# Performance work log

Measured on AMD Instinct MI355X. Metric: run time of the kernel, lower is better.

The kernel has to match this reference:

```python
import jax, jax.numpy as jnp
import numpy as np

SLOPE = 0.01  # LeakyReLU default negative slope


def grid_sample2d(image, grid):
    """Bilinear, padding_mode='border', align_corners=True.
    image: [B,C,H,W], grid: [B,h,w,2] in [-1,1]. Returns [B,C,h,w]."""
    B, C, H, W = image.shape
    _, h, w, _ = grid.shape
    ix = (grid[..., 0] + 1) / 2 * (W - 1)  # [B,h,w]
    iy = (grid[..., 1] + 1) / 2 * (H - 1)
    ix0 = jnp.floor(ix)
    iy0 = jnp.floor(iy)
    # bilinear weights (computed from unclamped corner coords, as in source)
    nw = (ix0 + 1 - ix) * (iy0 + 1 - iy)
    ne = (ix - ix0) * (iy0 + 1 - iy)
    sw = (ix0 + 1 - ix) * (iy - iy0)
    se = (ix - ix0) * (iy - iy0)
    x0 = jnp.clip(ix0.astype(jnp.int32), 0, W - 1)
    x1 = jnp.clip(ix0.astype(jnp.int32) + 1, 0, W - 1)
    y0 = jnp.clip(iy0.astype(jnp.int32), 0, H - 1)
    y1 = jnp.clip(iy0.astype(jnp.int32) + 1, 0, H - 1)
    img = image.reshape(B, C, H * W)

    def gather(yi, xi):
        idx = (yi * W + xi).reshape(B, 1, h * w)
        idx = jnp.broadcast_to(idx, (B, C, h * w))
        return jnp.take_along_axis(img, idx, axis=2).reshape(B, C, h, w)

    out = (gather(y0, x0) * nw[:, None] + gather(y0, x1) * ne[:, None]
           + gather(y1, x0) * sw[:, None] + gather(y1, x1) * se[:, None])
    return out


def leaky_relu(x):
    return jnp.where(x >= 0, x, SLOPE * x)


def setup_inputs() -> dict:
    key = jax.random.key(0)
    ks = jax.random.split(key, 10)
    B, C, H, W = 1, 32, 512, 512
    h, w = 2048, 512
    hid, out_dim = 32, 4
    inp = {
        "xy": jax.random.normal(ks[0], (B, C, H, W), jnp.float32),
        "xz": jax.random.normal(ks[1], (B, C, H, W), jnp.float32),
        "yz": jax.random.normal(ks[2], (B, C, H, W), jnp.float32),
        "coords": jax.random.uniform(ks[3], (B, h, w, 3), jnp.float32, -1.0, 1.0),
        "gauss_mat": jax.random.normal(ks[4], (3, 16), jnp.float32),
        "W0": jax.random.normal(ks[5], (C + 32, C), jnp.float32) * 0.1,
        "b0": jnp.zeros((C,), jnp.float32),
        "W1": jax.random.normal(ks[6], (C, hid), jnp.float32) * 0.1,
        "b1": jnp.zeros((hid,), jnp.float32),
        "W2": jax.random.normal(ks[7], (hid, hid), jnp.float32) * 0.1,
        "b2": jnp.zeros((hid,), jnp.float32),
        "W3": jax.random.normal(ks[8], (hid, out_dim), jnp.float32) * 0.1,
        "b3": jnp.zeros((out_dim,), jnp.float32),
    }
    return inp


def reference(xy, xz, yz, coords, gauss_mat, W0, b0, W1, b1, W2, b2, W3, b3):
    e1 = grid_sample2d(xy, coords[..., jnp.array([0, 1])])
    e2 = grid_sample2d(xz, coords[..., jnp.array([0, 2])])
    e3 = grid_sample2d(yz, coords[..., jnp.array([1, 2])])
    x = (e1 + e2 + e3) / 3.0  # [B,C,h,w]
    x = jnp.moveaxis(x, 1, -1)  # [B,h,w,C]
    # positional encoding
    p = coords * (2.0 * jnp.pi)
    proj = jnp.einsum('bhwd,dc->bhwc', p, gauss_mat)  # [B,h,w,16]
    pos_emb = jnp.concatenate([jnp.sin(proj), jnp.cos(proj)], axis=-1)  # [B,h,w,32]
    x = leaky_relu(jnp.concatenate([x, pos_emb], axis=-1) @ W0 + b0)
    x = leaky_relu(x @ W1 + b1)
    x = leaky_relu(x @ W2 + b2)
    x = x @ W3 + b3
    return x
```

## Files before the change

kernel.cpp:

```cpp
#include <hip/hip_runtime.h>
#include <hip/hip_fp16.h>

#define HW_ (512 * 512)
#define NPIX (2048 * 512)
#define NBIN 4096
#define SORT_BLOCKS 256
#define PXPT 16

typedef _Float16 half_t;
typedef __attribute__((ext_vector_type(8))) _Float16 half8;
typedef __attribute__((ext_vector_type(2))) _Float16 half2v;
typedef __attribute__((ext_vector_type(4))) float f32x4;
typedef unsigned int uint;

__device__ __forceinline__ half8 splat8(float w)
{
    half_t h = (half_t)w;
    half8 r = {h, h, h, h, h, h, h, h};
    return r;
}

__device__ __forceinline__ uint packh(float lo, float hi)
{
    half_t l = (half_t)lo, h = (half_t)hi;
    unsigned short lb = __builtin_bit_cast(unsigned short, l);
    unsigned short hb = __builtin_bit_cast(unsigned short, h);
    return (uint)lb | ((uint)hb << 16);
}

__device__ __forceinline__ uint pkrtz_u32(float lo, float hi)
{
    return __builtin_bit_cast(uint, __builtin_amdgcn_cvt_pkrtz(lo, hi));
}

__device__ __forceinline__ float lky(float x) { return x >= 0.f ? x : 0.01f * x; }

__device__ __forceinline__ uint pk_lky_u32(float a, float b)
{
    uint h = pkrtz_u32(a, b);
    half2v v = __builtin_bit_cast(half2v, h);
    half2v c = {(half_t)0.01f, (half_t)0.01f};
    half2v m = __builtin_elementwise_max(v, v * c);
    return __builtin_bit_cast(uint, m);
}

__device__ __forceinline__ unsigned spread4(int v)
{
    return (v & 1) | ((v & 2) << 2) | ((v & 4) << 4) | ((v & 8) << 6);
}

__device__ __forceinline__ unsigned bin_of(float cx, float cy, float cz)
{
    int qx = min(max((int)((cx + 1.f) * 8.f), 0), 15);
    int qy = min(max((int)((cy + 1.f) * 8.f), 0), 15);
    int qz = min(max((int)((cz + 1.f) * 8.f), 0), 15);
    return spread4(qx) | (spread4(qy) << 1) | (spread4(qz) << 2);
}

__global__ __launch_bounds__(256) void big_k(
    const float* __restrict__ xy, const float* __restrict__ xz,
    const float* __restrict__ yz, half_t* __restrict__ tp,
    const float* __restrict__ coords, unsigned* __restrict__ hist,
    const float* __restrict__ W0, const float* __restrict__ W1,
    const float* __restrict__ W2, const float* __restrict__ W3,
    const float* __restrict__ b0, const float* __restrict__ b1,
    const float* __restrict__ b2, const float* __restrict__ b3,
    uint* __restrict__ wfrag, float* __restrict__ bb)
{
    __shared__ __align__(16) uint sh[4096];
    int b = blockIdx.x;
    int t = threadIdx.x;

    if (b < 12288) {
        half_t (*tile)[68] = (half_t(*)[68])sh;
        int xc = b & 7;
        int y  = (b >> 3) & 511;
        int p  = b >> 12;
        const float* __restrict__ src = (p == 0) ? xy : (p == 1) ? xz : yz;
#pragma unroll
        for (int i = 0; i < 8; ++i) {
            int e  = i * 256 + t;
            int c  = e >> 6;
            int xl = e & 63;
            tile[c][xl] = (half_t)src[(size_t)c * HW_ + y * 512 + xc * 64 + xl];
        }
        __syncthreads();
        half_t* __restrict__ dst = tp + ((size_t)p * HW_ + y * 512 + xc * 64) * 32;
#pragma unroll
        for (int i = 0; i < 8; ++i) {
            int e  = i * 256 + t;
            int c  = e & 31;
            int xl = e >> 5;
            dst[(size_t)xl * 32 + c] = tile[c][xl];
        }
    } else if (b < 12288 + SORT_BLOCKS) {
        uint* lcnt = sh;
#pragma unroll
        for (int i = 0; i < NBIN / 256; ++i) lcnt[i * 256 + t] = 0;
        __syncthreads();
        int base = (b - 12288) * (PXPT * 256);
#pragma unroll
        for (int i = 0; i < PXPT; ++i) {
            int px = base + i * 256 + t;
            float cx = coords[(size_t)px * 3 + 0];
            float cy = coords[(size_t)px * 3 + 1];
            float cz = coords[(size_t)px * 3 + 2];
            atomicAdd(&lcnt[bin_of(cx, cy, cz)], 1u);
        }
        __syncthreads();
#pragma unroll
        for (int i = 0; i < NBIN / 256; ++i) {
            uint v = lcnt[i * 256 + t];
            if (v) atomicAdd(&hist[i * 256 + t], v);
        }
    } else {
        int tid = (b - 12288 - SORT_BLOCKS) * 256 + t;
        if (tid < 2304) {
            int f = tid >> 8, rem = tid & 255;
            int l = rem >> 2, u = rem & 3;
            int jl = l & 15, g = l >> 4;
            float lo, hi;
            if (f < 4) {
                int t_ = f >> 1, c = f & 1;
                int j  = t_ * 16 + jl;
                int k0 = 32 * c + 8 * g + 2 * u;
                float sc = c ? 1.f : (1.f / 3.f);
                lo = W0[k0 * 32 + j] * sc;
                hi = W0[(k0 + 1) * 32 + j] * sc;
            } else if (f < 8) {
                const float* W = (f < 6) ? W1 : W2;
                int t_ = f & 1;
                int j  = t_ * 16 + jl;
                int klo = (u < 2) ? (4 * g + 2 * u) : (16 + 4 * g + 2 * u - 4);
                lo = W[klo * 32 + j];
                hi = W[(klo + 1) * 32 + j];
            } else {
                int klo = (u < 2) ? (4 * g + 2 * u) : (16 + 4 * g + 2 * u - 4);
                lo = (jl < 4) ? W3[klo * 4 + jl] : 0.f;
                hi = (jl < 4) ? W3[(klo + 1) * 4 + jl] : 0.f;
            }
            wfrag[tid] = packh(lo, hi);
        } else if (tid < 2304 + 112) {
            int u = tid - 2304;
            float v;
            if (u < 32)      v = b0[u];
            else if (u < 64) v = b1[u - 32];
            else if (u < 96) v = b2[u - 64];
            else             v = (u - 96 < 4) ? b3[u - 96] : 0.f;
            bb[u] = v;
        }
    }
}

__global__ __launch_bounds__(256) void scan_k(const unsigned* __restrict__ hist,
                                              unsigned* __restrict__ ofs)
{
    __shared__ unsigned part[256];
    int t = threadIdx.x;
    unsigned loc[16], s = 0;
#pragma unroll
    for (int i = 0; i < 16; ++i) { loc[i] = s; s += hist[t * 16 + i]; }
    part[t] = s;
    __syncthreads();
    for (int d = 1; d < 256; d <<= 1) {
        unsigned v = (t >= d) ? part[t - d] : 0u;
        __syncthreads();
        part[t] += v;
        __syncthreads();
    }
    unsigned base = (t == 0) ? 0u : part[t - 1];
#pragma unroll
    for (int i = 0; i < 16; ++i) ofs[t * 16 + i] = base + loc[i];
}

__global__ __launch_bounds__(256) void scatter_k(const float* __restrict__ coords,
                                                 unsigned* __restrict__ ofs,
                                                 float4* __restrict__ sorted)
{
    __shared__ unsigned lcnt[NBIN];
    __shared__ unsigned lbase[NBIN];
    int t = threadIdx.x;
#pragma unroll
    for (int i = 0; i < NBIN / 256; ++i) lcnt[i * 256 + t] = 0;
    __syncthreads();

    int base = blockIdx.x * (PXPT * 256);
    float cxv[PXPT], cyv[PXPT], czv[PXPT];
    uint sav[PXPT];
#pragma unroll
    for (int i = 0; i < PXPT; ++i) {
        int px = base + i * 256 + t;
        cxv[i] = coords[(size_t)px * 3 + 0];
        cyv[i] = coords[(size_t)px * 3 + 1];
        czv[i] = coords[(size_t)px * 3 + 2];
        unsigned bn = bin_of(cxv[i], cyv[i], czv[i]);
        unsigned r  = atomicAdd(&lcnt[bn], 1u);
        sav[i] = (bn << 16) | r;
    }
    __syncthreads();
#pragma unroll
    for (int i = 0; i < NBIN / 256; ++i) {
        uint v = lcnt[i * 256 + t];
        lbase[i * 256 + t] = v ? atomicAdd(&ofs[i * 256 + t], v) : 0u;
    }
    __syncthreads();

#pragma unroll
    for (int i = 0; i < PXPT; ++i) {
        int px = base + i * 256 + t;
        unsigned bn = sav[i] >> 16, r = sav[i] & 0xffffu;
        sorted[lbase[bn] + r] = make_float4(cxv[i], cyv[i], czv[i],
                                            __uint_as_float((uint)px));
    }
}

__device__ __forceinline__ void axis1d(float gc, int& i0, int& i1, float& tf)
{
    float ic = fmaf(gc, 255.5f, 255.5f);
    float fc = floorf(ic);
    tf = ic - fc;
    int c0 = (int)fc;
    i0 = min(max(c0, 0), 511);
    i1 = min(max(c0 + 1, 0), 511);
}

__device__ __forceinline__ void interp_q(const half_t* __restrict__ pl,
                                         int i00, int i01, int i10, int i11,
                                         float tc, float tr, int ch, half8& acc)
{
    const half_t* __restrict__ p = pl + ch * 8;
    half8 a = *(const half8*)(p + (size_t)i00 * 32);
    half8 b = *(const half8*)(p + (size_t)i01 * 32);
    half8 c = *(const half8*)(p + (size_t)i10 * 32);
    half8 d = *(const half8*)(p + (size_t)i11 * 32);
    float w00 = (1.f - tc) * (1.f - tr);
    float w01 = tc * (1.f - tr);
    float w10 = (1.f - tc) * tr;
    float w11 = tc * tr;
    acc = acc + a * splat8(w00) + b * splat8(w01) + c * splat8(w10) + d * splat8(w11);
}

__device__ __forceinline__ void corners(float gx, float gy,
                                        int& i00, int& i01, int& i10, int& i11,
                                        float& wnw, float& wne, float& wsw, float& wse)
{
    int x0, x1, y0, y1; float tx, ty;
    axis1d(gx, x0, x1, tx);
    axis1d(gy, y0, y1, ty);
    i00 = y0 * 512 + x0;
    i01 = y0 * 512 + x1;
    i10 = y1 * 512 + x0;
    i11 = y1 * 512 + x1;
    wnw = (1.f - tx) * (1.f - ty);
    wne = tx * (1.f - ty);
    wsw = (1.f - tx) * ty;
    wse = tx * ty;
}

__global__ __launch_bounds__(128) void decoder_fused_k(
    const half_t* __restrict__ tp, const float4* __restrict__ sorted,
    const float* __restrict__ gauss, const uint* __restrict__ wfrag,
    const float* __restrict__ bb, float* __restrict__ out)
{
    __shared__ __align__(16) char act0[2][8192];
    const int t  = threadIdx.x;
    const int l  = t & 63;
    const int wv = t >> 6;
    char* base = act0[wv];
    const int jl = l & 15, g = l >> 4;
    const int ch = l & 3;
    const int pq = l >> 2;

    int b   = blockIdx.x;
    int swz = (b & 7) * 1024 + (b >> 3);
    int j   = (swz * 2 + wv) * 64 + l;

    float4 s = sorted[j];
    uint idreg = __float_as_uint(s.w);
    float cx = s.x, cy = s.y, cz = s.z;

#pragma unroll
    for (int q = 0; q < 4; ++q) {
        int pp = q * 16 + pq;
        float gx = __shfl(cx, pp);
        float gy = __shfl(cy, pp);
        float gz = __shfl(cz, pp);
        int x0, x1, y0, y1, z0, z1;
        float tx, ty, tz;
        axis1d(gx, x0, x1, tx);
        axis1d(gy, y0, y1, ty);
        axis1d(gz, z0, z1, tz);
        half8 accq = {};
        interp_q(tp,
                 y0 * 512 + x0, y0 * 512 + x1, y1 * 512 + x0, y1 * 512 + x1,
                 tx, ty, ch, accq);
        interp_q(tp + (size_t)HW_ * 32,
                 z0 * 512 + x0, z0 * 512 + x1, z1 * 512 + x0, z1 * 512 + x1,
                 tx, tz, ch, accq);
        interp_q(tp + (size_t)2 * HW_ * 32,
                 z0 * 512 + y0, z0 * 512 + y1, z1 * 512 + y0, z1 * 512 + y1,
                 ty, tz, ch, accq);
        *(half8*)(base + (pp << 7) + ((ch ^ (pp & 7)) << 4)) = accq;
    }

    half8 wf[9];
#pragma unroll
    for (int f = 0; f < 9; ++f) {
        uint4 u = *(const uint4*)(wfrag + f * 256 + l * 4);
        wf[f] = __builtin_bit_cast(half8, u);
    }
    f32x4 bv0a = *(const f32x4*)(bb +  0 + g * 4);
    f32x4 bv0b = *(const f32x4*)(bb + 16 + g * 4);
    f32x4 bv1a = *(const f32x4*)(bb + 32 + g * 4);
    f32x4 bv1b = *(const f32x4*)(bb + 48 + g * 4);
    f32x4 bv2a = *(const f32x4*)(bb + 64 + g * 4);
    f32x4 bv2b = *(const f32x4*)(bb + 80 + g * 4);
    f32x4 bv3  = *(const f32x4*)(bb + 96 + g * 4);

    const float TWO_PI = 6.283185307179586f;
    float px = cx * TWO_PI, py = cy * TWO_PI, pz = cz * TWO_PI;
    float sn[16], cs[16];
#pragma unroll
    for (int c = 0; c < 16; ++c) {
        float pr = px * gauss[c] + py * gauss[16 + c] + pz * gauss[32 + c];
        sn[c] = __sinf(pr);
        cs[c] = __cosf(pr);
    }
    half8 pc[4];
#pragma unroll
    for (int i = 0; i < 8; ++i) {
        pc[0][i] = (half_t)sn[i];     pc[1][i] = (half_t)sn[8 + i];
        pc[2][i] = (half_t)cs[i];     pc[3][i] = (half_t)cs[8 + i];
    }
#pragma unroll
    for (int c = 0; c < 4; ++c)
        *(half8*)(base + (l << 7) + (((4 + c) ^ (l & 7)) << 4)) = pc[c];

#pragma unroll
    for (int pt = 0; pt < 4; ++pt) {
        int p = pt * 16 + jl;
        half8 Ba = *(const half8*)(base + (p << 7) + ((g ^ (p & 7)) << 4));
        half8 Bb = *(const half8*)(base + (p << 7) + (((4 + g) ^ (p & 7)) << 4));

        f32x4 d0 = bv0a, d1 = bv0b;
        d0 = __builtin_amdgcn_mfma_f32_16x16x32_f16(wf[0], Ba, d0, 0, 0, 0);
        d0 = __builtin_amdgcn_mfma_f32_16x16x32_f16(wf[1], Bb, d0, 0, 0, 0);
        d1 = __builtin_amdgcn_mfma_f32_16x16x32_f16(wf[2], Ba, d1, 0, 0, 0);
        d1 = __builtin_amdgcn_mfma_f32_16x16x32_f16(wf[3], Bb, d1, 0, 0, 0);
        uint4 u1;
        u1.x = pk_lky_u32(d0[0], d0[1]);
        u1.y = pk_lky_u32(d0[2], d0[3]);
        u1.z = pk_lky_u32(d1[0], d1[1]);
        u1.w = pk_lky_u32(d1[2], d1[3]);
        half8 B1 = __builtin_bit_cast(half8, u1);

        d0 = bv1a; d1 = bv1b;
        d0 = __builtin_amdgcn_mfma_f32_16x16x32_f16(wf[4], B1, d0, 0, 0, 0);
        d1 = __builtin_amdgcn_mfma_f32_16x16x32_f16(wf[5], B1, d1, 0, 0, 0);
        uint4 u2;
        u2.x = pk_lky_u32(d0[0], d0[1]);
        u2.y = pk_lky_u32(d0[2], d0[3]);
        u2.z = pk_lky_u32(d1[0], d1[1]);
        u2.w = pk_lky_u32(d1[2], d1[3]);
        half8 B2 = __builtin_bit_cast(half8, u2);

        d0 = bv2a; d1 = bv2b;
        d0 = __builtin_amdgcn_mfma_f32_16x16x32_f16(wf[6], B2, d0, 0, 0, 0);
        d1 = __builtin_amdgcn_mfma_f32_16x16x32_f16(wf[7], B2, d1, 0, 0, 0);
        uint4 u3;
        u3.x = pk_lky_u32(d0[0], d0[1]);
        u3.y = pk_lky_u32(d0[2], d0[3]);
        u3.z = pk_lky_u32(d1[0], d1[1]);
        u3.w = pk_lky_u32(d1[2], d1[3]);
        half8 B3 = __builtin_bit_cast(half8, u3);

        f32x4 d3 = bv3;
        d3 = __builtin_amdgcn_mfma_f32_16x16x32_f16(wf[8], B3, d3, 0, 0, 0);
        int gid = __shfl((int)idreg, pt * 16 + (l & 15));
        if (l < 16) {
            *(f32x4*)(out + (size_t)(uint)gid * 4) = d3;
        }
    }
}

__device__ __forceinline__ void sample_dir(const float* __restrict__ pl,
                                           float gx, float gy, float* __restrict__ acc)
{
    int i00, i01, i10, i11;
    float wnw, wne, wsw, wse;
    corners(gx, gy, i00, i01, i10, i11, wnw, wne, wsw, wse);
#pragma unroll
    for (int c = 0; c < 32; ++c) {
        const float* __restrict__ bq = pl + (size_t)c * HW_;
        acc[c] += wnw * bq[i00] + wne * bq[i01] + wsw * bq[i10] + wse * bq[i11];
    }
}

__global__ __launch_bounds__(256) void decoder_fb_k(
    const float* __restrict__ xy, const float* __restrict__ xz,
    const float* __restrict__ yz,
    const float* __restrict__ coords, const float* __restrict__ gauss,
    const float* __restrict__ W0, const float* __restrict__ b0,
    const float* __restrict__ W1, const float* __restrict__ b1,
    const float* __restrict__ W2, const float* __restrict__ b2,
    const float* __restrict__ W3, const float* __restrict__ b3,
    float* __restrict__ out)
{
    int pix = blockIdx.x * 256 + threadIdx.x;
    float cx = coords[(size_t)pix * 3 + 0];
    float cy = coords[(size_t)pix * 3 + 1];
    float cz = coords[(size_t)pix * 3 + 2];

    float act[64];
#pragma unroll
    for (int i = 0; i < 32; ++i) act[i] = 0.f;
    sample_dir(xy, cx, cy, act);
    sample_dir(xz, cx, cz, act);
    sample_dir(yz, cy, cz, act);
#pragma unroll
    for (int i = 0; i < 32; ++i) act[i] *= (1.f / 3.f);

    const float TWO_PI = 6.283185307179586f;
    float px = cx * TWO_PI, py = cy * TWO_PI, pz = cz * TWO_PI;
#pragma unroll
    for (int c = 0; c < 16; ++c) {
        float pr = px * gauss[c] + py * gauss[16 + c] + pz * gauss[32 + c];
        act[32 + c] = __sinf(pr);
        act[48 + c] = __cosf(pr);
    }

    float h[32];
#pragma unroll
    for (int jj = 0; jj < 32; ++jj) h[jj] = b0[jj];
#pragma unroll
    for (int k = 0; k < 64; ++k) {
        float a = act[k];
#pragma unroll
        for (int jj = 0; jj < 32; ++jj) h[jj] = fmaf(a, W0[k * 32 + jj], h[jj]);
    }
#pragma unroll
    for (int jj = 0; jj < 32; ++jj) act[jj] = lky(h[jj]);
#pragma unroll
    for (int jj = 0; jj < 32; ++jj) h[jj] = b1[jj];
#pragma unroll
    for (int k = 0; k < 32; ++k) {
        float a = act[k];
#pragma unroll
        for (int jj = 0; jj < 32; ++jj) h[jj] = fmaf(a, W1[k * 32 + jj], h[jj]);
    }
#pragma unroll
    for (int jj = 0; jj < 32; ++jj) act[jj] = lky(h[jj]);
#pragma unroll
    for (int jj = 0; jj < 32; ++jj) h[jj] = b2[jj];
#pragma unroll
    for (int k = 0; k < 32; ++k) {
        float a = act[k];
#pragma unroll
        for (int jj = 0; jj < 32; ++jj) h[jj] = fmaf(a, W2[k * 32 + jj], h[jj]);
    }
#pragma unroll
    for (int jj = 0; jj < 32; ++jj) act[jj] = lky(h[jj]);
    float o[4];
#pragma unroll
    for (int jj = 0; jj < 4; ++jj) o[jj] = b3[jj];
#pragma unroll
    for (int k = 0; k < 32; ++k) {
        float a = act[k];
#pragma unroll
        for (int jj = 0; jj < 4; ++jj) o[jj] = fmaf(a, W3[k * 4 + jj], o[jj]);
    }
    *(float4*)(out + (size_t)pix * 4) = make_float4(o[0], o[1], o[2], o[3]);
}

extern "C" void kernel_launch(void* const* d_in, const int* in_sizes, int n_in,
                              void* d_out, int out_size, void* d_ws, size_t ws_size,
                              hipStream_t stream)
{
    const float* xy     = (const float*)d_in[0];
    const float* xz     = (const float*)d_in[1];
    const float* yz     = (const float*)d_in[2];
    const float* coords = (const float*)d_in[3];
    const float* gauss  = (const float*)d_in[4];
    const float* W0     = (const float*)d_in[5];
    const float* b0     = (const float*)d_in[6];
    const float* W1     = (const float*)d_in[7];
    const float* b1     = (const float*)d_in[8];
    const float* W2     = (const float*)d_in[9];
    const float* b2     = (const float*)d_in[10];
    const float* W3     = (const float*)d_in[11];
    const float* b3     = (const float*)d_in[12];
    float* out = (float*)d_out;

    const size_t plane_bytes = (size_t)3 * HW_ * 32 * sizeof(half_t);
    const size_t hist_off    = plane_bytes;
    const size_t ofs_off     = hist_off + NBIN * 4;
    const size_t wfrag_off   = ofs_off + NBIN * 4;
    const size_t bb_off      = wfrag_off + 12288;
    const size_t sorted_off  = bb_off + 4096;
    const size_t need_fused  = sorted_off + (size_t)NPIX * sizeof(float4);

    if (ws_size >= need_fused) {
        half_t*   tp     = (half_t*)d_ws;
        unsigned* hist   = (unsigned*)((char*)d_ws + hist_off);
        unsigned* ofs    = (unsigned*)((char*)d_ws + ofs_off);
        uint*     wfrag  = (uint*)((char*)d_ws + wfrag_off);
        float*    bb     = (float*)((char*)d_ws + bb_off);
        float4*   sorted = (float4*)((char*)d_ws + sorted_off);

        (void)hipMemsetAsync(hist, 0, NBIN * 4, stream);
        big_k<<<12288 + SORT_BLOCKS + 10, 256, 0, stream>>>(
            xy, xz, yz, tp, coords, hist,
            W0, W1, W2, W3, b0, b1, b2, b3, wfrag, bb);
        scan_k<<<1, 256, 0, stream>>>(hist, ofs);
        scatter_k<<<SORT_BLOCKS, 256, 0, stream>>>(coords, ofs, sorted);
        decoder_fused_k<<<NPIX / 128, 128, 0, stream>>>(
            tp, sorted, gauss, wfrag, bb, out);
    } else {
        decoder_fb_k<<<NPIX / 256, 256, 0, stream>>>(
            xy, xz, yz, coords, gauss,
            W0, b0, W1, b1, W2, b2, W3, b3, out);
    }
}
```

Before: 137.3 us.

## Interleave gather passes with MLP tiles and pass activations via shuffles

Removes the per-wave 8KB LDS activation buffer: gathered features now move into MFMA B-operand layout through lane shuffles, and the positional encoding is computed per tile directly in registers. Gather passes are interleaved with MLP tiles in a software-pipelined order, so that gather memory latency can overlap with MFMA work. Biases are staged in a small shared array behind a block barrier. The trade-offs are more shuffle instructions, recomputing sin/cos per lane group, and higher register pressure from holding two gather results at once.

```diff
diff --git a/kernel.cpp b/kernel.cpp
--- a/kernel.cpp
+++ b/kernel.cpp
@@ -257,16 +257,118 @@
     wse = tx * ty;
 }
 
+__device__ __forceinline__ half8 gather_pass(const half_t* __restrict__ tp,
+                                             float cx, float cy, float cz,
+                                             int q, int pq, int ch)
+{
+    int pp = q * 16 + pq;
+    float gx = __shfl(cx, pp);
+    float gy = __shfl(cy, pp);
+    float gz = __shfl(cz, pp);
+    int x0, x1, y0, y1, z0, z1;
+    float tx, ty, tz;
+    axis1d(gx, x0, x1, tx);
+    axis1d(gy, y0, y1, ty);
+    axis1d(gz, z0, z1, tz);
+    half8 acc = {};
+    interp_q(tp,
+             y0 * 512 + x0, y0 * 512 + x1, y1 * 512 + x0, y1 * 512 + x1,
+             tx, ty, ch, acc);
+    interp_q(tp + (size_t)HW_ * 32,
+             z0 * 512 + x0, z0 * 512 + x1, z1 * 512 + x0, z1 * 512 + x1,
+             tx, tz, ch, acc);
+    interp_q(tp + (size_t)2 * HW_ * 32,
+             z0 * 512 + y0, z0 * 512 + y1, z1 * 512 + y0, z1 * 512 + y1,
+             ty, tz, ch, acc);
+    return acc;
+}
+
+__device__ __forceinline__ void mlp_tile(
+    int pt, half8 accv, float cx, float cy, float cz, uint idreg,
+    const half8* __restrict__ wf, const float* __restrict__ sbb,
+    const float* __restrict__ gauss, int l, int jl, int g,
+    float* __restrict__ out)
+{
+    const float TWO_PI = 6.283185307179586f;
+
+    uint4 av = __builtin_bit_cast(uint4, accv);
+    int srcl = 4 * jl + g;
+    uint4 bu;
+    bu.x = (uint)__shfl((int)av.x, srcl);
+    bu.y = (uint)__shfl((int)av.y, srcl);
+    bu.z = (uint)__shfl((int)av.z, srcl);
+    bu.w = (uint)__shfl((int)av.w, srcl);
+    half8 Ba = __builtin_bit_cast(half8, bu);
+
+    int p = pt * 16 + jl;
+    float sx = __shfl(cx, p) * TWO_PI;
+    float sy = __shfl(cy, p) * TWO_PI;
+    float sz = __shfl(cz, p) * TWO_PI;
+    const int c0 = 8 * (g & 1);
+    half8 Bb;
+#pragma unroll
+    for (int i = 0; i < 8; ++i) {
+        float pr = sx * gauss[c0 + i] + sy * gauss[16 + c0 + i]
+                 + sz * gauss[32 + c0 + i];
+        float v = (g < 2) ? __sinf(pr) : __cosf(pr);
+        Bb[i] = (half_t)v;
+    }
+
+    f32x4 d0 = *(const f32x4*)(sbb +  0 + g * 4);
+    f32x4 d1 = *(const f32x4*)(sbb + 16 + g * 4);
+    d0 = __builtin_amdgcn_mfma_f32_16x16x32_f16(wf[0], Ba, d0, 0, 0, 0);
+    d0 = __builtin_amdgcn_mfma_f32_16x16x32_f16(wf[1], Bb, d0, 0, 0, 0);
+    d1 = __builtin_amdgcn_mfma_f32_16x16x32_f16(wf[2], Ba, d1, 0, 0, 0);
+    d1 = __builtin_amdgcn_mfma_f32_16x16x32_f16(wf[3], Bb, d1, 0, 0, 0);
+    uint4 u1;
+    u1.x = pk_lky_u32(d0[0], d0[1]);
+    u1.y = pk_lky_u32(d0[2], d0[3]);
+    u1.z = pk_lky_u32(d1[0], d1[1]);
+    u1.w = pk_lky_u32(d1[2], d1[3]);
+    half8 B1 = __builtin_bit_cast(half8, u1);
+
+    d0 = *(const f32x4*)(sbb + 32 + g * 4);
+    d1 = *(const f32x4*)(sbb + 48 + g * 4);
+    d0 = __builtin_amdgcn_mfma_f32_16x16x32_f16(wf[4], B1, d0, 0, 0, 0);
+    d1 = __builtin_amdgcn_mfma_f32_16x16x32_f16(wf[5], B1, d1, 0, 0, 0);
+    uint4 u2;
+    u2.x = pk_lky_u32(d0[0], d0[1]);
+    u2.y = pk_lky_u32(d0[2], d0[3]);
+    u2.z = pk_lky_u32(d1[0], d1[1]);
+    u2.w = pk_lky_u32(d1[2], d1[3]);
+    half8 B2 = __builtin_bit_cast(half8, u2);
+
+    d0 = *(const f32x4*)(sbb + 64 + g * 4);
+    d1 = *(const f32x4*)(sbb + 80 + g * 4);
+    d0 = __builtin_amdgcn_mfma_f32_16x16x32_f16(wf[6], B2, d0, 0, 0, 0);
+    d1 = __builtin_amdgcn_mfma_f32_16x16x32_f16(wf[7], B2, d1, 0, 0, 0);
+    uint4 u3;
+    u3.x = pk_lky_u32(d0[0], d0[1]);
+    u3.y = pk_lky_u32(d0[2], d0[3]);
+    u3.z = pk_lky_u32(d1[0], d1[1]);
+    u3.w = pk_lky_u32(d1[2], d1[3]);
+    half8 B3 = __builtin_bit_cast(half8, u3);
+
+    f32x4 d3 = *(const f32x4*)(sbb + 96 + g * 4);
+    d3 = __builtin_amdgcn_mfma_f32_16x16x32_f16(wf[8], B3, d3, 0, 0, 0);
+    int gid = __shfl((int)idreg, pt * 16 + (l & 15));
+    if (l < 16) {
+        *(f32x4*)(out + (size_t)(uint)gid * 4) = d3;
+    }
+}
+
 __global__ __launch_bounds__(128) void decoder_fused_k(
     const half_t* __restrict__ tp, const float4* __restrict__ sorted,
     const float* __restrict__ gauss, const uint* __restrict__ wfrag,
     const float* __restrict__ bb, float* __restrict__ out)
 {
-    __shared__ __align__(16) char act0[2][8192];
+    __shared__ __align__(16) float sbb[112];
     const int t  = threadIdx.x;
+    if (t < 112) sbb[t] = bb[t];
+    __syncthreads();
+
     const int l  = t & 63;
     const int wv = t >> 6;
-    char* base = act0[wv];
     const int jl = l & 15, g = l >> 4;
     const int ch = l & 3;
     const int pq = l >> 2;
@@ -279,108 +381,21 @@
     uint idreg = __float_as_uint(s.w);
     float cx = s.x, cy = s.y, cz = s.z;
 
-#pragma unroll
-    for (int q = 0; q < 4; ++q) {
-        int pp = q * 16 + pq;
-        float gx = __shfl(cx, pp);
-        float gy = __shfl(cy, pp);
-        float gz = __shfl(cz, pp);
-        int x0, x1, y0, y1, z0, z1;
-        float tx, ty, tz;
-        axis1d(gx, x0, x1, tx);
-        axis1d(gy, y0, y1, ty);
-        axis1d(gz, z0, z1, tz);
-        half8 accq = {};
-        interp_q(tp,
-                 y0 * 512 + x0, y0 * 512 + x1, y1 * 512 + x0, y1 * 512 + x1,
-                 tx, ty, ch, accq);
-        interp_q(tp + (size_t)HW_ * 32,
-                 z0 * 512 + x0, z0 * 512 + x1, z1 * 512 + x0, z1 * 512 + x1,
-                 tx, tz, ch, accq);
-        interp_q(tp + (size_t)2 * HW_ * 32,
-                 z0 * 512 + y0, z0 * 512 + y1, z1 * 512 + y0, z1 * 512 + y1,
-                 ty, tz, ch, accq);
-        *(half8*)(base + (pp << 7) + ((ch ^ (pp & 7)) << 4)) = accq;
-    }
-
     half8 wf[9];
 #pragma unroll
     for (int f = 0; f < 9; ++f) {
         uint4 u = *(const uint4*)(wfrag + f * 256 + l * 4);
         wf[f] = __builtin_bit_cast(half8, u);
     }
-    f32x4 bv0a = *(const f32x4*)(bb +  0 + g * 4);
-    f32x4 bv0b = *(const f32x4*)(bb + 16 + g * 4);
-    f32x4 bv1a = *(const f32x4*)(bb + 32 + g * 4);
-    f32x4 bv1b = *(const f32x4*)(bb + 48 + g * 4);
-    f32x4 bv2a = *(const f32x4*)(bb + 64 + g * 4);
-    f32x4 bv2b = *(const f32x4*)(bb + 80 + g * 4);
-    f32x4 bv3  = *(const f32x4*)(bb + 96 + g * 4);
-
-    const float TWO_PI = 6.283185307179586f;
-    float px = cx * TWO_PI, py = cy * TWO_PI, pz = cz * TWO_PI;
-    float sn[16], cs[16];
-#pragma unroll
-    for (int c = 0; c < 16; ++c) {
-        float pr = px * gauss[c] + py * gauss[16 + c] + pz * gauss[32 + c];
-        sn[c] = __sinf(pr);
-        cs[c] = __cosf(pr);
-    }
-    half8 pc[4];
-#pragma unroll
-    for (int i = 0; i < 8; ++i) {
-        pc[0][i] = (half_t)sn[i];     pc[1][i] = (half_t)sn[8 + i];
-        pc[2][i] = (half_t)cs[i];     pc[3][i] = (half_t)cs[8 + i];
-    }
-#pragma unroll
-    for (int c = 0; c < 4; ++c)
-        *(half8*)(base + (l << 7) + (((4 + c) ^ (l & 7)) << 4)) = pc[c];
-
-#pragma unroll
-    for (int pt = 0; pt < 4; ++pt) {
-        int p = pt * 16 + jl;
-        half8 Ba = *(const half8*)(base + (p << 7) + ((g ^ (p & 7)) << 4));
-        half8 Bb = *(const half8*)(base + (p << 7) + (((4 + g) ^ (p & 7)) << 4));
-
-        f32x4 d0 = bv0a, d1 = bv0b;
-        d0 = __builtin_amdgcn_mfma_f32_16x16x32_f16(wf[0], Ba, d0, 0, 0, 0);
-        d0 = __builtin_amdgcn_mfma_f32_16x16x32_f16(wf[1], Bb, d0, 0, 0, 0);
-        d1 = __builtin_amdgcn_mfma_f32_16x16x32_f16(wf[2], Ba, d1, 0, 0, 0);
-        d1 = __builtin_amdgcn_mfma_f32_16x16x32_f16(wf[3], Bb, d1, 0, 0, 0);
-        uint4 u1;
-        u1.x = pk_lky_u32(d0[0], d0[1]);
-        u1.y = pk_lky_u32(d0[2], d0[3]);
-        u1.z = pk_lky_u32(d1[0], d1[1]);
-        u1.w = pk_lky_u32(d1[2], d1[3]);
-        half8 B1 = __builtin_bit_cast(half8, u1);
-
-        d0 = bv1a; d1 = bv1b;
-        d0 = __builtin_amdgcn_mfma_f32_16x16x32_f16(wf[4], B1, d0, 0, 0, 0);
-        d1 = __builtin_amdgcn_mfma_f32_16x16x32_f16(wf[5], B1, d1, 0, 0, 0);
-        uint4 u2;
-        u2.x = pk_lky_u32(d0[0], d0[1]);
-        u2.y = pk_lky_u32(d0[2], d0[3]);
-        u2.z = pk_lky_u32(d1[0], d1[1]);
-        u2.w = pk_lky_u32(d1[2], d1[3]);
-        half8 B2 = __builtin_bit_cast(half8, u2);
-
-        d0 = bv2a; d1 = bv2b;
-        d0 = __builtin_amdgcn_mfma_f32_16x16x32_f16(wf[6], B2, d0, 0, 0, 0);
-        d1 = __builtin_amdgcn_mfma_f32_16x16x32_f16(wf[7], B2, d1, 0, 0, 0);
-        uint4 u3;
-        u3.x = pk_lky_u32(d0[0], d0[1]);
-        u3.y = pk_lky_u32(d0[2], d0[3]);
-        u3.z = pk_lky_u32(d1[0], d1[1]);
-        u3.w = pk_lky_u32(d1[2], d1[3]);
-        half8 B3 = __builtin_bit_cast(half8, u3);
-
-        f32x4 d3 = bv3;
-        d3 = __builtin_amdgcn_mfma_f32_16x16x32_f16(wf[8], B3, d3, 0, 0, 0);
-        int gid = __shfl((int)idreg, pt * 16 + (l & 15));
-        if (l < 16) {
-            *(f32x4*)(out + (size_t)(uint)gid * 4) = d3;
-        }
-    }
+
+    half8 a0 = gather_pass(tp, cx, cy, cz, 0, pq, ch);
+    half8 a1 = gather_pass(tp, cx, cy, cz, 1, pq, ch);
+    mlp_tile(0, a0, cx, cy, cz, idreg, wf, sbb, gauss, l, jl, g, out);
+    half8 a2 = gather_pass(tp, cx, cy, cz, 2, pq, ch);
+    mlp_tile(1, a1, cx, cy, cz, idreg, wf, sbb, gauss, l, jl, g, out);
+    half8 a3 = gather_pass(tp, cx, cy, cz, 3, pq, ch);
+    mlp_tile(2, a2, cx, cy, cz, idreg, wf, sbb, gauss, l, jl, g, out);
+    mlp_tile(3, a3, cx, cy, cz, idreg, wf, sbb, gauss, l, jl, g, out);
 }
 
 __device__ __forceinline__ void sample_dir(const float* __restrict__ pl,
```

Result: no change. 136.2 us (-0.8%).
